# Optimization experiments

Measured on AMD Instinct MI355X. Metric: run time of the kernel, lower is better.

## Reference

```python
import jax, jax.numpy as jnp
import numpy as np

B, S, D, H = 2, 2048, 1024, 16
HD = D // H  # head_dim = 64

def setup_inputs() -> dict:
    key = jax.random.key(0)
    ks = jax.random.split(key, 10)
    s = 1.0 / np.sqrt(D)
    return {
        "hidden_states": jax.random.normal(ks[0], (B, S, D), jnp.float32),
        "attention_mask": jnp.ones((B, S), jnp.float32),
        "q_w": jax.random.uniform(ks[1], (D, D), jnp.float32, -s, s),
        "q_b": jax.random.uniform(ks[2], (D,), jnp.float32, -s, s),
        "k_w": jax.random.uniform(ks[3], (D, D), jnp.float32, -s, s),
        "k_b": jax.random.uniform(ks[4], (D,), jnp.float32, -s, s),
        "v_w": jax.random.uniform(ks[5], (D, D), jnp.float32, -s, s),
        "v_b": jax.random.uniform(ks[6], (D,), jnp.float32, -s, s),
        "o_w": jax.random.uniform(ks[7], (D, D), jnp.float32, -s, s),
        "o_b": jax.random.uniform(ks[8], (D,), jnp.float32, -s, s),
    }

def reference(hidden_states, attention_mask, q_w, q_b, k_w, k_b, v_w, v_b, o_w, o_b):
    scale = HD ** -0.5
    # projections; torch Linear: x @ W^T + b. Here weights stored as (D, D) used directly.
    q = hidden_states @ q_w + q_b  # [B,S,D]
    k = hidden_states @ k_w + k_b
    v = hidden_states @ v_w + v_b
    # split heads -> [B,H,S,HD]
    q = q.reshape(B, S, H, HD).transpose(0, 2, 1, 3)
    k = k.reshape(B, S, H, HD).transpose(0, 2, 1, 3)
    v = v.reshape(B, S, H, HD).transpose(0, 2, 1, 3)
    scores = jnp.einsum('bhqd,bhkd->bhqk', q, k) * scale  # [B,H,S,S]
    # additive mask from 2D [B,S] mask (1=keep, 0=mask)
    scores = scores + (1.0 - attention_mask)[:, None, None, :] * -10000.0
    attn = jax.nn.softmax(scores, axis=-1)
    ctx = jnp.einsum('bhqk,bhkd->bhqd', attn, v)  # [B,H,S,HD]
    ctx = ctx.transpose(0, 2, 1, 3).reshape(B, S, D)
    return ctx @ o_w + o_b
```

## Files before the change

### kernel.cpp

```cpp
#include <hip/hip_runtime.h>
#include <hip/hip_bf16.h>

#define B_ 2
#define S_ 2048
#define D_ 1024
#define H_ 16
#define HD_ 64

#define QSCALE 0.18033688f
#define MLOG2E 14426.950408f

#define EXP2(x) __builtin_amdgcn_exp2f(x)

typedef __attribute__((ext_vector_type(8))) short bf16x8;
typedef __attribute__((ext_vector_type(4))) short short4v;
typedef __attribute__((ext_vector_type(4))) float floatx4;

static __device__ __forceinline__ float bf2f(short u) {
  union { float f; unsigned int i; } c;
  c.i = ((unsigned int)(unsigned short)u) << 16;
  return c.f;
}
static __device__ __forceinline__ short f2bf(float f) {
  union { float f; unsigned int i; } c; c.f = f;
  unsigned int r = c.i + 0x7FFFu + ((c.i >> 16) & 1u);
  return (short)(r >> 16);
}
static __device__ __forceinline__ short f2bf_fast(float f) {
  union { float f; unsigned int i; } c; c.f = f;
  return (short)((c.i + 0x8000u) >> 16);
}

static __device__ __forceinline__ void gld_lds16(const void* g, void* l) {
  __builtin_amdgcn_global_load_lds(
      (const __attribute__((address_space(1))) unsigned int*)g,
      (__attribute__((address_space(3))) unsigned int*)l, 16, 0, 0);
}

__global__ __launch_bounds__(256)
void prep(const float* __restrict__ w0, const float* __restrict__ w1,
          const float* __restrict__ w2, const float* __restrict__ w3,
          const float* __restrict__ hs, short* __restrict__ WT,
          short* __restrict__ Xb) {
  const int z = blockIdx.z;
  if (z < 4) {
    __shared__ short t[64][65];
    const float* src = z == 0 ? w0 : z == 1 ? w1 : z == 2 ? w2 : w3;
    short* dst = WT + (size_t)z * D_ * D_;
    const int tx = threadIdx.x & 63, ty = threadIdx.x >> 6;
    const int r0 = blockIdx.y * 64, c0 = blockIdx.x * 64;
    for (int r = ty; r < 64; r += 4)
      t[r][tx] = f2bf(src[(size_t)(r0 + r) * D_ + c0 + tx]);
    __syncthreads();
    for (int r = ty; r < 64; r += 4)
      dst[(size_t)(c0 + r) * D_ + r0 + tx] = t[tx][r];
  } else {
    const int bid = blockIdx.y * 16 + blockIdx.x;
    const float4* in4 = (const float4*)hs;
    short4v* out4 = (short4v*)Xb;
#pragma unroll
    for (int i = 0; i < 16; i++) {
      const int idx = bid * 4096 + i * 256 + threadIdx.x;
      const float4 v = in4[idx];
      short4v o;
      o[0] = f2bf(v.x); o[1] = f2bf(v.y); o[2] = f2bf(v.z); o[3] = f2bf(v.w);
      out4[idx] = o;
    }
  }
}

__global__ __launch_bounds__(256, 2)
void gemm_qkv(const short* __restrict__ X, const short* __restrict__ WT,
              const float* __restrict__ qb, const float* __restrict__ kb,
              const float* __restrict__ vb, const float* __restrict__ mask,
              short* __restrict__ Qo, short* __restrict__ Ko,
              short* __restrict__ Vt) {
  __shared__ __align__(16) short As[128 * 32];
  __shared__ __align__(16) short Bs[128 * 32];
  const int tid = threadIdx.x;
  const int wave = tid >> 6, lane = tid & 63;
  const int col = lane & 15, quad = lane >> 4;
  const int m0 = blockIdx.x * 128;
  const int nt = blockIdx.y;
  const int widx = nt >> 3;
  const int n1 = (nt & 7) * 128;
  const short* Bsrc = WT + (size_t)widx * D_ * D_ + (size_t)n1 * D_;
  const int b = m0 >> 11;

  const int srow = tid >> 2;
  const int skcol = (tid & 3) * 8;
  const short* ga = X + (size_t)(m0 + srow) * D_ + skcol;
  const short* gb = Bsrc + (size_t)srow * D_ + skcol;
  short* la = As + tid * 8;
  short* lb = Bs + tid * 8;

  floatx4 acc[4][4];
#pragma unroll
  for (int i = 0; i < 4; i++)
#pragma unroll
    for (int j = 0; j < 4; j++) acc[i][j] = floatx4{0.f, 0.f, 0.f, 0.f};

  if (widx < 2) {
    const int wseq = (wave >> 1) * 64;
    const int wfeat = (wave & 1) * 64;
    for (int k0 = 0; k0 < D_; k0 += 32) {
      gld_lds16(ga, la);
      gld_lds16(ga + 64 * D_, la + 2048);
      gld_lds16(gb, lb);
      gld_lds16(gb + 64 * D_, lb + 2048);
      ga += 32; gb += 32;
      __syncthreads();
      bf16x8 xf[4], wf[4];
#pragma unroll
      for (int j = 0; j < 4; j++)
        xf[j] = *(const bf16x8*)(As + (wseq + j * 16 + col) * 32 + quad * 8);
#pragma unroll
      for (int i = 0; i < 4; i++)
        wf[i] = *(const bf16x8*)(Bs + (wfeat + i * 16 + col) * 32 + quad * 8);
#pragma unroll
      for (int i = 0; i < 4; i++)
#pragma unroll
        for (int j = 0; j < 4; j++)
          acc[i][j] = __builtin_amdgcn_mfma_f32_16x16x32_bf16(wf[i], xf[j],
                                                              acc[i][j], 0, 0, 0);
      __syncthreads();
    }
    const float* bias = widx == 0 ? qb : kb;
    short* dst = widx == 0 ? Qo : Ko;
    const float scale = widx == 0 ? QSCALE : 1.0f;
#pragma unroll
    for (int i = 0; i < 4; i++) {
      const int nf = n1 + wfeat + i * 16 + quad * 4;
      const int h = nf >> 6, hd = nf & 63;
      const float4 bv = *(const float4*)(bias + nf);
#pragma unroll
      for (int j = 0; j < 4; j++) {
        const int s = (m0 + wseq + j * 16 + col) & (S_ - 1);
        short4v pk;
        pk[0] = f2bf((acc[i][j][0] + bv.x) * scale);
        pk[1] = f2bf((acc[i][j][1] + bv.y) * scale);
        pk[2] = f2bf((acc[i][j][2] + bv.z) * scale);
        pk[3] = f2bf((acc[i][j][3] + bv.w) * scale);
        *(short4v*)(dst + ((size_t)(b * H_ + h) * S_ + s) * HD_ + hd) = pk;
      }
    }
  } else {
    const int wrow = (wave & 1) * 64;
    const int wcol = (wave >> 1) * 64;
    for (int k0 = 0; k0 < D_; k0 += 32) {
      gld_lds16(ga, la);
      gld_lds16(ga + 64 * D_, la + 2048);
      gld_lds16(gb, lb);
      gld_lds16(gb + 64 * D_, lb + 2048);
      ga += 32; gb += 32;
      __syncthreads();
      bf16x8 af[4], bfr[4];
#pragma unroll
      for (int i = 0; i < 4; i++)
        af[i] = *(const bf16x8*)(As + (wrow + i * 16 + col) * 32 + quad * 8);
#pragma unroll
      for (int j = 0; j < 4; j++)
        bfr[j] = *(const bf16x8*)(Bs + (wcol + j * 16 + col) * 32 + quad * 8);
#pragma unroll
      for (int i = 0; i < 4; i++)
#pragma unroll
        for (int j = 0; j < 4; j++)
          acc[i][j] = __builtin_amdgcn_mfma_f32_16x16x32_bf16(af[i], bfr[j],
                                                              acc[i][j], 0, 0, 0);
      __syncthreads();
    }
    float bv[4];
#pragma unroll
    for (int j = 0; j < 4; j++) bv[j] = vb[n1 + wcol + j * 16 + col];
    const float* mkb = mask + (size_t)b * S_;
#pragma unroll
    for (int i = 0; i < 4; i++) {
      const int s = (m0 + wrow + i * 16 + quad * 4) & (S_ - 1);
      const float4 mv = *(const float4*)(mkb + s);
      float w[4];
      w[0] = EXP2((mv.x - 1.0f) * MLOG2E);
      w[1] = EXP2((mv.y - 1.0f) * MLOG2E);
      w[2] = EXP2((mv.z - 1.0f) * MLOG2E);
      w[3] = EXP2((mv.w - 1.0f) * MLOG2E);
#pragma unroll
      for (int j = 0; j < 4; j++) {
        const int nl = n1 + wcol + j * 16 + col;
        const int h = nl >> 6, hd = nl & 63;
        short4v pk;
#pragma unroll
        for (int r = 0; r < 4; r++) pk[r] = f2bf((acc[i][j][r] + bv[j]) * w[r]);
        *(short4v*)(Vt + ((size_t)(b * H_ + h) * HD_ + hd) * S_ + s) = pk;
      }
    }
  }
}

__global__ __launch_bounds__(256, 2)
void attn(const short* __restrict__ Q, const short* __restrict__ K,
          const short* __restrict__ Vt, const float* __restrict__ mask,
          short* __restrict__ ctx) {
  __shared__ __align__(16) short Ks[2][4096];
  __shared__ __align__(16) short Vs[2][4096];
  __shared__ __align__(16) short P[4][2][16][68];
  __shared__ __align__(16) short Ws[S_];
  const int tid = threadIdx.x, wave = tid >> 6, lane = tid & 63;
  const int col = lane & 15, quad = lane >> 4;
  const int lin = blockIdx.x;
  const int qt = (lin >> 3) & 15;
  const int gi = (lin & 7) + ((lin >> 7) << 3);
  const int h = gi & 15, b = gi >> 4;
  const short* Qh = Q + (size_t)(b * H_ + h) * S_ * HD_;
  const short* Kh = K + (size_t)(b * H_ + h) * S_ * HD_;
  const short* Vh = Vt + (size_t)(b * H_ + h) * HD_ * S_;
  const float* mk = mask + (size_t)b * S_;
  const int q0 = qt * 128 + wave * 32;

  const int r1 = tid >> 3, c1 = (tid & 7) ^ (r1 & 7);
  const int r2 = r1 + 32,  c2 = (tid & 7) ^ (r2 & 7);
  const int swz = quad ^ (col & 7);

  gld_lds16(Kh + (size_t)r1 * HD_ + c1 * 8, &Ks[0][tid * 8]);
  gld_lds16(Kh + (size_t)r2 * HD_ + c2 * 8, &Ks[0][(tid + 256) * 8]);
  gld_lds16(Vh + (size_t)r1 * S_ + c1 * 8, &Vs[0][tid * 8]);
  gld_lds16(Vh + (size_t)r2 * S_ + c2 * 8, &Vs[0][(tid + 256) * 8]);

  for (int i = tid; i < S_; i += 256)
    Ws[i] = f2bf(EXP2((mk[i] - 1.0f) * MLOG2E));

  bf16x8 qf[2][2];
#pragma unroll
  for (int g = 0; g < 2; g++) {
    const short* qp = Qh + (size_t)(q0 + g * 16 + col) * HD_;
    qf[g][0] = *(const bf16x8*)(qp + quad * 8);
    qf[g][1] = *(const bf16x8*)(qp + 32 + quad * 8);
  }

  floatx4 acc[2][4], rsacc[2];
#pragma unroll
  for (int g = 0; g < 2; g++) {
    rsacc[g] = floatx4{0.f, 0.f, 0.f, 0.f};
#pragma unroll
    for (int d = 0; d < 4; d++) acc[g][d] = floatx4{0.f, 0.f, 0.f, 0.f};
  }

  __syncthreads();

  for (int it = 0; it < S_ / 64; it++) {
    const int buf = it & 1;
    const int kt = it * 64;
    if (it + 1 < S_ / 64) {
      const int kn = kt + 64;
      gld_lds16(Kh + (size_t)(kn + r1) * HD_ + c1 * 8, &Ks[buf ^ 1][tid * 8]);
      gld_lds16(Kh + (size_t)(kn + r2) * HD_ + c2 * 8, &Ks[buf ^ 1][(tid + 256) * 8]);
      gld_lds16(Vh + (size_t)r1 * S_ + kn + c1 * 8, &Vs[buf ^ 1][tid * 8]);
      gld_lds16(Vh + (size_t)r2 * S_ + kn + c2 * 8, &Vs[buf ^ 1][(tid + 256) * 8]);
    }

    bf16x8 kf[4][2];
#pragma unroll
    for (int t = 0; t < 4; t++) {
      const short* kp = &Ks[buf][(t * 16 + col) * 64];
      kf[t][0] = *(const bf16x8*)(kp + swz * 8);
      kf[t][1] = *(const bf16x8*)(kp + (swz ^ 4) * 8);
    }

#pragma unroll
    for (int g = 0; g < 2; g++)
#pragma unroll
      for (int t = 0; t < 4; t++) {
        floatx4 z = floatx4{0.f, 0.f, 0.f, 0.f};
        z = __builtin_amdgcn_mfma_f32_16x16x32_bf16(kf[t][0], qf[g][0], z, 0, 0, 0);
        z = __builtin_amdgcn_mfma_f32_16x16x32_bf16(kf[t][1], qf[g][1], z, 0, 0, 0);
        short4v pk;
#pragma unroll
        for (int r = 0; r < 4; r++) pk[r] = f2bf_fast(EXP2(z[r]));
        *(short4v*)&P[wave][g][col][t * 16 + quad * 4] = pk;
      }

    bf16x8 pf[2][2];
#pragma unroll
    for (int g = 0; g < 2; g++)
#pragma unroll
      for (int kk = 0; kk < 2; kk++)
        pf[g][kk] = *(const bf16x8*)&P[wave][g][col][kk * 32 + quad * 8];

    bf16x8 wf[2];
#pragma unroll
    for (int kk = 0; kk < 2; kk++)
      wf[kk] = *(const bf16x8*)&Ws[kt + kk * 32 + quad * 8];

#pragma unroll
    for (int g = 0; g < 2; g++) {
      rsacc[g] = __builtin_amdgcn_mfma_f32_16x16x32_bf16(wf[0], pf[g][0], rsacc[g], 0, 0, 0);
      rsacc[g] = __builtin_amdgcn_mfma_f32_16x16x32_bf16(wf[1], pf[g][1], rsacc[g], 0, 0, 0);
    }
#pragma unroll
    for (int d = 0; d < 4; d++) {
      const short* vp = &Vs[buf][(d * 16 + col) * 64];
      const bf16x8 vf0 = *(const bf16x8*)(vp + swz * 8);
      const bf16x8 vf1 = *(const bf16x8*)(vp + (swz ^ 4) * 8);
#pragma unroll
      for (int g = 0; g < 2; g++) {
        acc[g][d] = __builtin_amdgcn_mfma_f32_16x16x32_bf16(vf0, pf[g][0], acc[g][d], 0, 0, 0);
        acc[g][d] = __builtin_amdgcn_mfma_f32_16x16x32_bf16(vf1, pf[g][1], acc[g][d], 0, 0, 0);
      }
    }
    __syncthreads();
  }

#pragma unroll
  for (int g = 0; g < 2; g++) {
    const float inv = 1.0f / (rsacc[g][0] + 1e-30f);
    const size_t row = (size_t)b * S_ + q0 + g * 16 + col;
#pragma unroll
    for (int d = 0; d < 4; d++) {
      short4v o;
#pragma unroll
      for (int r = 0; r < 4; r++) o[r] = f2bf(acc[g][d][r] * inv);
      *(short4v*)(ctx + row * D_ + h * HD_ + d * 16 + quad * 4) = o;
    }
  }
}

__global__ __launch_bounds__(256, 2)
void gemm_out(const short* __restrict__ X, const short* __restrict__ WT,
              const float* __restrict__ ob, float* __restrict__ out) {
  __shared__ __align__(16) short As[64 * 32];
  __shared__ __align__(16) short Bs[128 * 32];
  const int tid = threadIdx.x;
  const int wave = tid >> 6, lane = tid & 63;
  const int col = lane & 15, quad = lane >> 4;
  const int m0 = blockIdx.x * 64;
  const int n0 = blockIdx.y * 128;
  const short* Bsrc = WT + (size_t)n0 * D_;
  const int wrow = (wave & 1) * 32;
  const int wcol = (wave >> 1) * 64;

  floatx4 acc[2][4];
#pragma unroll
  for (int i = 0; i < 2; i++)
#pragma unroll
    for (int j = 0; j < 4; j++) acc[i][j] = floatx4{0.f, 0.f, 0.f, 0.f};

  const int arow = tid >> 2, akcol = (tid & 3) * 8;
  const short* ga = X + (size_t)(m0 + arow) * D_ + akcol;
  const short* gb = Bsrc + (size_t)arow * D_ + akcol;
  short* la = As + tid * 8;
  short* lb = Bs + tid * 8;

  for (int k0 = 0; k0 < D_; k0 += 32) {
    gld_lds16(ga, la);
    gld_lds16(gb, lb);
    gld_lds16(gb + 64 * D_, lb + 2048);
    ga += 32; gb += 32;
    __syncthreads();
    bf16x8 af[2], bfr[4];
#pragma unroll
    for (int i = 0; i < 2; i++)
      af[i] = *(const bf16x8*)(As + (wrow + i * 16 + col) * 32 + quad * 8);
#pragma unroll
    for (int j = 0; j < 4; j++)
      bfr[j] = *(const bf16x8*)(Bs + (wcol + j * 16 + col) * 32 + quad * 8);
#pragma unroll
    for (int i = 0; i < 2; i++)
#pragma unroll
      for (int j = 0; j < 4; j++)
        acc[i][j] = __builtin_amdgcn_mfma_f32_16x16x32_bf16(af[i], bfr[j],
                                                            acc[i][j], 0, 0, 0);
    __syncthreads();
  }

  float bv[4];
#pragma unroll
  for (int j = 0; j < 4; j++) bv[j] = ob[n0 + wcol + j * 16 + col];

#pragma unroll
  for (int i = 0; i < 2; i++) {
    const int m = m0 + wrow + i * 16 + quad * 4;
#pragma unroll
    for (int j = 0; j < 4; j++) {
      const int n = n0 + wcol + j * 16 + col;
#pragma unroll
      for (int r = 0; r < 4; r++)
        out[(size_t)(m + r) * D_ + n] = acc[i][j][r] + bv[j];
    }
  }
}

extern "C" void kernel_launch(void* const* d_in, const int* in_sizes, int n_in,
                              void* d_out, int out_size, void* d_ws, size_t ws_size,
                              hipStream_t stream) {
  (void)in_sizes; (void)n_in; (void)out_size; (void)ws_size;
  const float* hs  = (const float*)d_in[0];
  const float* msk = (const float*)d_in[1];
  const float* qw  = (const float*)d_in[2];
  const float* qb  = (const float*)d_in[3];
  const float* kw  = (const float*)d_in[4];
  const float* kb  = (const float*)d_in[5];
  const float* vw  = (const float*)d_in[6];
  const float* vb  = (const float*)d_in[7];
  const float* ow  = (const float*)d_in[8];
  const float* ob  = (const float*)d_in[9];
  float* out = (float*)d_out;
  char* ws = (char*)d_ws;

  short* Xb  = (short*)(ws);
  short* WT  = (short*)(ws + (8ull  << 20));
  short* Qp  = (short*)(ws + (16ull << 20));
  short* Kp  = (short*)(ws + (24ull << 20));
  short* Vtp = (short*)(ws + (32ull << 20));
  short* Ctx = Xb;

  prep<<<dim3(16, 16, 5), 256, 0, stream>>>(qw, kw, vw, ow, hs, WT, Xb);
  gemm_qkv<<<dim3(32, 24), 256, 0, stream>>>(Xb, WT, qb, kb, vb, msk, Qp, Kp, Vtp);
  attn<<<dim3(512), 256, 0, stream>>>(Qp, Kp, Vtp, msk, Ctx);
  gemm_out<<<dim3(64, 8), 256, 0, stream>>>(Ctx, WT + 3ull * D_ * D_, ob, out);
}
```

Before: 195.9 us.

## Rewrite attention inner loop with 32x32 MFMA and register-resident probabilities

Switches the attention kernel from 16x16x32 to 32x32x16 bf16 MFMA tiles. The probability tile now stays in registers, rearranged with v_cvt_pk_bf16_f32 and v_permlane32_swap, instead of round-tripping through an LDS P buffer. The additive mask bias is folded into the QK accumulator init rather than applied as a multiplicative weight on V in the QKV GEMM, and row sums come from an MFMA against a ones vector. This removes LDS traffic and conversion work, at the cost of more accumulator registers and inline asm that depends on the gfx950 ISA.

Result: no change. 195.5 us (-0.2%).

```diff
diff --git a/kernel.cpp b/kernel.cpp
--- a/kernel.cpp
+++ b/kernel.cpp
@@ -15,6 +15,7 @@
 typedef __attribute__((ext_vector_type(8))) short bf16x8;
 typedef __attribute__((ext_vector_type(4))) short short4v;
 typedef __attribute__((ext_vector_type(4))) float floatx4;
+typedef __attribute__((ext_vector_type(16))) float f32x16;
 
 static __device__ __forceinline__ float bf2f(short u) {
   union { float f; unsigned int i; } c;
@@ -26,9 +27,14 @@
   unsigned int r = c.i + 0x7FFFu + ((c.i >> 16) & 1u);
   return (short)(r >> 16);
 }
-static __device__ __forceinline__ short f2bf_fast(float f) {
-  union { float f; unsigned int i; } c; c.f = f;
-  return (short)((c.i + 0x8000u) >> 16);
+
+static __device__ __forceinline__ int cvtpk_bf16(float a, float b) {
+  int r;
+  asm("v_cvt_pk_bf16_f32 %0, %1, %2" : "=v"(r) : "v"(a), "v"(b));
+  return r;
+}
+static __device__ __forceinline__ void swap32(int& a, int& b) {
+  asm("v_permlane32_swap_b32 %0, %1" : "+v"(a), "+v"(b));
 }
 
 static __device__ __forceinline__ void gld_lds16(const void* g, void* l) {
@@ -72,7 +78,7 @@
 __global__ __launch_bounds__(256, 2)
 void gemm_qkv(const short* __restrict__ X, const short* __restrict__ WT,
               const float* __restrict__ qb, const float* __restrict__ kb,
-              const float* __restrict__ vb, const float* __restrict__ mask,
+              const float* __restrict__ vb,
               short* __restrict__ Qo, short* __restrict__ Ko,
               short* __restrict__ Vt) {
   __shared__ __align__(16) short As[128 * 32];
@@ -172,23 +178,16 @@
     float bv[4];
 #pragma unroll
     for (int j = 0; j < 4; j++) bv[j] = vb[n1 + wcol + j * 16 + col];
-    const float* mkb = mask + (size_t)b * S_;
 #pragma unroll
     for (int i = 0; i < 4; i++) {
       const int s = (m0 + wrow + i * 16 + quad * 4) & (S_ - 1);
-      const float4 mv = *(const float4*)(mkb + s);
-      float w[4];
-      w[0] = EXP2((mv.x - 1.0f) * MLOG2E);
-      w[1] = EXP2((mv.y - 1.0f) * MLOG2E);
-      w[2] = EXP2((mv.z - 1.0f) * MLOG2E);
-      w[3] = EXP2((mv.w - 1.0f) * MLOG2E);
 #pragma unroll
       for (int j = 0; j < 4; j++) {
         const int nl = n1 + wcol + j * 16 + col;
         const int h = nl >> 6, hd = nl & 63;
         short4v pk;
 #pragma unroll
-        for (int r = 0; r < 4; r++) pk[r] = f2bf((acc[i][j][r] + bv[j]) * w[r]);
+        for (int r = 0; r < 4; r++) pk[r] = f2bf(acc[i][j][r] + bv[j]);
         *(short4v*)(Vt + ((size_t)(b * H_ + h) * HD_ + hd) * S_ + s) = pk;
       }
     }
@@ -201,10 +200,9 @@
           short* __restrict__ ctx) {
   __shared__ __align__(16) short Ks[2][4096];
   __shared__ __align__(16) short Vs[2][4096];
-  __shared__ __align__(16) short P[4][2][16][68];
-  __shared__ __align__(16) short Ws[S_];
+  __shared__ __align__(16) float Wb[S_];
   const int tid = threadIdx.x, wave = tid >> 6, lane = tid & 63;
-  const int col = lane & 15, quad = lane >> 4;
+  const int l31 = lane & 31, hi = lane >> 5, x7 = l31 & 7;
   const int lin = blockIdx.x;
   const int qt = (lin >> 3) & 15;
   const int gi = (lin & 7) + ((lin >> 7) << 3);
@@ -217,7 +215,6 @@
 
   const int r1 = tid >> 3, c1 = (tid & 7) ^ (r1 & 7);
   const int r2 = r1 + 32,  c2 = (tid & 7) ^ (r2 & 7);
-  const int swz = quad ^ (col & 7);
 
   gld_lds16(Kh + (size_t)r1 * HD_ + c1 * 8, &Ks[0][tid * 8]);
   gld_lds16(Kh + (size_t)r2 * HD_ + c2 * 8, &Ks[0][(tid + 256) * 8]);
@@ -225,23 +222,27 @@
   gld_lds16(Vh + (size_t)r2 * S_ + c2 * 8, &Vs[0][(tid + 256) * 8]);
 
   for (int i = tid; i < S_; i += 256)
-    Ws[i] = f2bf(EXP2((mk[i] - 1.0f) * MLOG2E));
-
-  bf16x8 qf[2][2];
-#pragma unroll
-  for (int g = 0; g < 2; g++) {
-    const short* qp = Qh + (size_t)(q0 + g * 16 + col) * HD_;
-    qf[g][0] = *(const bf16x8*)(qp + quad * 8);
-    qf[g][1] = *(const bf16x8*)(qp + 32 + quad * 8);
-  }
-
-  floatx4 acc[2][4], rsacc[2];
-#pragma unroll
-  for (int g = 0; g < 2; g++) {
-    rsacc[g] = floatx4{0.f, 0.f, 0.f, 0.f};
-#pragma unroll
-    for (int d = 0; d < 4; d++) acc[g][d] = floatx4{0.f, 0.f, 0.f, 0.f};
-  }
+    Wb[i] = (mk[i] - 1.0f) * MLOG2E;
+
+  bf16x8 qf[4];
+  {
+    const short* qp = Qh + (size_t)(q0 + l31) * HD_ + hi * 8;
+#pragma unroll
+    for (int c = 0; c < 4; c++) qf[c] = *(const bf16x8*)(qp + c * 16);
+  }
+
+  bf16x8 ones;
+#pragma unroll
+  for (int i = 0; i < 8; i++) ones[i] = (short)0x3F80;
+
+  f32x16 acc0, acc1, rsa;
+#pragma unroll
+  for (int r = 0; r < 16; r++) { acc0[r] = 0.f; acc1[r] = 0.f; rsa[r] = 0.f; }
+
+  const int kbase = l31 * 64;
+  int ko[4];
+#pragma unroll
+  for (int c = 0; c < 4; c++) ko[c] = ((((c << 1) | hi) ^ x7) << 3);
 
   __syncthreads();
 
@@ -256,69 +257,70 @@
       gld_lds16(Vh + (size_t)r2 * S_ + kn + c2 * 8, &Vs[buf ^ 1][(tid + 256) * 8]);
     }
 
-    bf16x8 kf[4][2];
-#pragma unroll
-    for (int t = 0; t < 4; t++) {
-      const short* kp = &Ks[buf][(t * 16 + col) * 64];
-      kf[t][0] = *(const bf16x8*)(kp + swz * 8);
-      kf[t][1] = *(const bf16x8*)(kp + (swz ^ 4) * 8);
-    }
-
-#pragma unroll
-    for (int g = 0; g < 2; g++)
-#pragma unroll
-      for (int t = 0; t < 4; t++) {
-        floatx4 z = floatx4{0.f, 0.f, 0.f, 0.f};
-        z = __builtin_amdgcn_mfma_f32_16x16x32_bf16(kf[t][0], qf[g][0], z, 0, 0, 0);
-        z = __builtin_amdgcn_mfma_f32_16x16x32_bf16(kf[t][1], qf[g][1], z, 0, 0, 0);
-        short4v pk;
-#pragma unroll
-        for (int r = 0; r < 4; r++) pk[r] = f2bf_fast(EXP2(z[r]));
-        *(short4v*)&P[wave][g][col][t * 16 + quad * 4] = pk;
+    bf16x8 pB[4];
+#pragma unroll
+    for (int t = 0; t < 2; t++) {
+      const int kb2 = kt + t * 32 + 4 * hi;
+      const float4 b0 = *(const float4*)&Wb[kb2];
+      const float4 b1 = *(const float4*)&Wb[kb2 + 8];
+      const float4 b2 = *(const float4*)&Wb[kb2 + 16];
+      const float4 b3 = *(const float4*)&Wb[kb2 + 24];
+      f32x16 z;
+      z[0] = b0.x; z[1] = b0.y; z[2]  = b0.z; z[3]  = b0.w;
+      z[4] = b1.x; z[5] = b1.y; z[6]  = b1.z; z[7]  = b1.w;
+      z[8] = b2.x; z[9] = b2.y; z[10] = b2.z; z[11] = b2.w;
+      z[12] = b3.x; z[13] = b3.y; z[14] = b3.z; z[15] = b3.w;
+      const short* kp = &Ks[buf][t * 2048 + kbase];
+#pragma unroll
+      for (int c = 0; c < 4; c++) {
+        const bf16x8 kf = *(const bf16x8*)(kp + ko[c]);
+        z = __builtin_amdgcn_mfma_f32_32x32x16_bf16(kf, qf[c], z, 0, 0, 0);
       }
-
-    bf16x8 pf[2][2];
-#pragma unroll
-    for (int g = 0; g < 2; g++)
-#pragma unroll
-      for (int kk = 0; kk < 2; kk++)
-        pf[g][kk] = *(const bf16x8*)&P[wave][g][col][kk * 32 + quad * 8];
-
-    bf16x8 wf[2];
-#pragma unroll
-    for (int kk = 0; kk < 2; kk++)
-      wf[kk] = *(const bf16x8*)&Ws[kt + kk * 32 + quad * 8];
-
-#pragma unroll
-    for (int g = 0; g < 2; g++) {
-      rsacc[g] = __builtin_amdgcn_mfma_f32_16x16x32_bf16(wf[0], pf[g][0], rsacc[g], 0, 0, 0);
-      rsacc[g] = __builtin_amdgcn_mfma_f32_16x16x32_bf16(wf[1], pf[g][1], rsacc[g], 0, 0, 0);
-    }
-#pragma unroll
-    for (int d = 0; d < 4; d++) {
-      const short* vp = &Vs[buf][(d * 16 + col) * 64];
-      const bf16x8 vf0 = *(const bf16x8*)(vp + swz * 8);
-      const bf16x8 vf1 = *(const bf16x8*)(vp + (swz ^ 4) * 8);
-#pragma unroll
-      for (int g = 0; g < 2; g++) {
-        acc[g][d] = __builtin_amdgcn_mfma_f32_16x16x32_bf16(vf0, pf[g][0], acc[g][d], 0, 0, 0);
-        acc[g][d] = __builtin_amdgcn_mfma_f32_16x16x32_bf16(vf1, pf[g][1], acc[g][d], 0, 0, 0);
-      }
+      float p[16];
+#pragma unroll
+      for (int r = 0; r < 16; r++) p[r] = EXP2(z[r]);
+      int a0 = cvtpk_bf16(p[0], p[1]),   a1 = cvtpk_bf16(p[2], p[3]);
+      int cc0 = cvtpk_bf16(p[4], p[5]),  cc1 = cvtpk_bf16(p[6], p[7]);
+      int e0 = cvtpk_bf16(p[8], p[9]),   e1 = cvtpk_bf16(p[10], p[11]);
+      int g0 = cvtpk_bf16(p[12], p[13]), g1 = cvtpk_bf16(p[14], p[15]);
+      swap32(a0, cc0); swap32(a1, cc1);
+      swap32(e0, g0);  swap32(e1, g1);
+      union { int i[4]; bf16x8 v; } u0, u1;
+      u0.i[0] = a0; u0.i[1] = a1; u0.i[2] = cc0; u0.i[3] = cc1;
+      u1.i[0] = e0; u1.i[1] = e1; u1.i[2] = g0;  u1.i[3] = g1;
+      pB[t * 2] = u0.v;
+      pB[t * 2 + 1] = u1.v;
+    }
+
+#pragma unroll
+    for (int kc = 0; kc < 4; kc++)
+      rsa = __builtin_amdgcn_mfma_f32_32x32x16_bf16(ones, pB[kc], rsa, 0, 0, 0);
+
+    const short* vp0 = &Vs[buf][kbase];
+    const short* vp1 = &Vs[buf][2048 + kbase];
+#pragma unroll
+    for (int kc = 0; kc < 4; kc++) {
+      const bf16x8 vf0 = *(const bf16x8*)(vp0 + ko[kc]);
+      const bf16x8 vf1 = *(const bf16x8*)(vp1 + ko[kc]);
+      acc0 = __builtin_amdgcn_mfma_f32_32x32x16_bf16(vf0, pB[kc], acc0, 0, 0, 0);
+      acc1 = __builtin_amdgcn_mfma_f32_32x32x16_bf16(vf1, pB[kc], acc1, 0, 0, 0);
     }
     __syncthreads();
   }
 
-#pragma unroll
-  for (int g = 0; g < 2; g++) {
-    const float inv = 1.0f / (rsacc[g][0] + 1e-30f);
-    const size_t row = (size_t)b * S_ + q0 + g * 16 + col;
-#pragma unroll
-    for (int d = 0; d < 4; d++) {
-      short4v o;
-#pragma unroll
-      for (int r = 0; r < 4; r++) o[r] = f2bf(acc[g][d][r] * inv);
-      *(short4v*)(ctx + row * D_ + h * HD_ + d * 16 + quad * 4) = o;
-    }
+  const float inv = 1.0f / (rsa[0] + 1e-30f);
+  const size_t row = (size_t)b * S_ + q0 + l31;
+#pragma unroll
+  for (int g4 = 0; g4 < 4; g4++) {
+    short4v o0, o1;
+#pragma unroll
+    for (int j = 0; j < 4; j++) {
+      o0[j] = f2bf(acc0[g4 * 4 + j] * inv);
+      o1[j] = f2bf(acc1[g4 * 4 + j] * inv);
+    }
+    short* cp = ctx + row * D_ + h * HD_ + g4 * 8 + 4 * hi;
+    *(short4v*)(cp) = o0;
+    *(short4v*)(cp + 32) = o1;
   }
 }
 
@@ -412,7 +414,7 @@
   short* Ctx = Xb;
 
   prep<<<dim3(16, 16, 5), 256, 0, stream>>>(qw, kw, vw, ow, hs, WT, Xb);
-  gemm_qkv<<<dim3(32, 24), 256, 0, stream>>>(Xb, WT, qb, kb, vb, msk, Qp, Kp, Vtp);
+  gemm_qkv<<<dim3(32, 24), 256, 0, stream>>>(Xb, WT, qb, kb, vb, Qp, Kp, Vtp);
   attn<<<dim3(512), 256, 0, stream>>>(Qp, Kp, Vtp, msk, Ctx);
   gemm_out<<<dim3(64, 8), 256, 0, stream>>>(Ctx, WT + 3ull * D_ * D_, ob, out);
 }
```
